# Performance work log

Hardware: AMD Instinct MI355X
Metric: run time of the kernel (lower is better)

The kernel has to match this reference:

```python
import jax, jax.numpy as jnp
import numpy as np

D = 256
N_EDGES = 8192
N_CORNERS = 4096


def setup_inputs() -> dict:
    key = jax.random.key(0)
    ks = jax.random.split(key, 8)
    scale = 1.0 / np.sqrt(D)
    return {
        "edge_pred": jax.random.uniform(ks[0], (N_EDGES,), dtype=jnp.float32),
        "edge_corner": jax.random.randint(ks[1], (N_EDGES, 2), 0, N_CORNERS, dtype=jnp.int64),
        "all_corners": jax.random.uniform(ks[2], (N_CORNERS, 2), dtype=jnp.float32),
        "edge_x": jax.random.normal(ks[3], (N_EDGES, D), dtype=jnp.float32),
        "image_x": jax.random.normal(ks[4], (1024,), dtype=jnp.float32),
        "W1": jax.random.normal(ks[5], (D, D), dtype=jnp.float32) * scale,
        "b1": jnp.zeros((D,), dtype=jnp.float32),
        "W2": jax.random.normal(ks[6], (D, D), dtype=jnp.float32) * scale,
        "b2": jnp.zeros((D,), dtype=jnp.float32),
        "W3": jax.random.normal(ks[7], (3 * D, D), dtype=jnp.float32) * scale,
        "b3": jnp.zeros((D,), dtype=jnp.float32),
    }


def _linear_block(x, W, b):
    # LinearBlock: Linear followed by ReLU
    return jax.nn.relu(x @ W + b)


def reference(edge_pred, edge_corner, all_corners, edge_x, image_x, W1, b1, W2, b2, W3, b3):
    # 'fully' branch of MPModule.forward. edge_pred/edge_corner/all_corners/image_x
    # are unused in this branch (kept for signature fidelity).
    e1 = _linear_block(edge_x, W1, b1)              # [N, D]
    # (e1.unsqueeze(1) * e1).mean(-1) == (e1 @ e1.T) / D   -> [N, N]
    sim1 = (e1 @ e1.T) / D
    e2 = _linear_block(edge_x, W2, b2)
    sim2 = (e2 @ e2.T) / D
    # (edge_x * sim.unsqueeze(-1)).sum(1) == sim @ edge_x  -> [N, D]
    agg1 = sim1 @ edge_x
    agg2 = sim2 @ edge_x
    cat = jnp.concatenate([edge_x, agg1, agg2], axis=-1)  # [N, 3D]
    out = _linear_block(cat, W3, b3)                      # [N, D]
    return out
```

## Files before the change

kernel.cpp:

```cpp
#include <hip/hip_runtime.h>

#define NE 8192
#define DD 256
#define NSPLIT 16

typedef __attribute__((ext_vector_type(8))) short short8;
typedef __attribute__((ext_vector_type(4))) short short4v;
typedef __attribute__((ext_vector_type(8))) __bf16 bf16x8;
typedef __attribute__((ext_vector_type(4))) float floatx4;

__device__ __forceinline__ unsigned short f2bf(float f) {
  union { float f; unsigned int i; } v; v.f = f;
  unsigned int r = v.i + 0x7fffu + ((v.i >> 16) & 1u);
  return (unsigned short)(r >> 16);
}

__device__ __forceinline__ floatx4 mfma_bf16(short8 a, short8 b, floatx4 c) {
  return __builtin_amdgcn_mfma_f32_16x16x32_bf16(
      __builtin_bit_cast(bf16x8, a), __builtin_bit_cast(bf16x8, b), c, 0, 0, 0);
}

__global__ __launch_bounds__(256, 2)
void e_gemm(const float* __restrict__ x,
            const float* __restrict__ W1, const float* __restrict__ b1,
            const float* __restrict__ W2, const float* __restrict__ b2,
            unsigned short* __restrict__ e1, unsigned short* __restrict__ e2,
            unsigned short* __restrict__ e1T, unsigned short* __restrict__ e2T,
            unsigned short* __restrict__ xT)
{
  __shared__ __align__(16) unsigned short smA[128 * 136];
  __shared__ __align__(16) unsigned short smB[64 * 136];
  const int T = threadIdx.x, lane = T & 63, wv = T >> 6;
  const int q = lane >> 4, r = lane & 15;
  const int z = blockIdx.z;
  const int col0 = blockIdx.x * 64, row0 = blockIdx.y * 128;
  const float* W = z ? W2 : W1;
  const float* bi = z ? b2 : b1;
  unsigned short* eo = z ? e2 : e1;
  unsigned short* eoT = z ? e2T : e1T;
  const bool emit = (z == 0) && ((int)blockIdx.x == (int)(blockIdx.y & 3));
  const int wr = (wv >> 1) * 64, wc = (wv & 1) * 32;

  floatx4 acc[4][2];
#pragma unroll
  for (int i = 0; i < 4; ++i)
#pragma unroll
    for (int j = 0; j < 2; ++j) acc[i][j] = (floatx4){0.f, 0.f, 0.f, 0.f};

  for (int kc = 0; kc < 256; kc += 128) {
#pragma unroll
    for (int p = 0; p < 16; ++p) {
      const int id = p * 256 + T, rr = id >> 5, k4 = (id & 31) * 4;
      floatx4 v = *(const floatx4*)&x[(size_t)(row0 + rr) * DD + kc + k4];
      short4v s;
#pragma unroll
      for (int c = 0; c < 4; ++c) s[c] = (short)f2bf(v[c]);
      *(short4v*)&smA[rr * 136 + k4] = s;
    }
#pragma unroll
    for (int p = 0; p < 2; ++p) {
      const int id = p * 256 + T, kb = id >> 4, n4 = id & 15;
      floatx4 wrow[4];
#pragma unroll
      for (int i = 0; i < 4; ++i)
        wrow[i] = *(const floatx4*)&W[(size_t)(kc + kb * 4 + i) * DD + col0 + n4 * 4];
#pragma unroll
      for (int s4 = 0; s4 < 4; ++s4) {
        const int c = (s4 + n4) & 3;
        short4v sv = {(short)f2bf(wrow[0][c]), (short)f2bf(wrow[1][c]),
                      (short)f2bf(wrow[2][c]), (short)f2bf(wrow[3][c])};
        *(short4v*)&smB[(n4 * 4 + c) * 136 + kb * 4] = sv;
      }
    }
    __syncthreads();
#pragma unroll
    for (int ks = 0; ks < 4; ++ks) {
      short8 af[4], bf[2];
#pragma unroll
      for (int i = 0; i < 4; ++i)
        af[i] = *(const short8*)&smA[(wr + i * 16 + r) * 136 + ks * 32 + q * 8];
#pragma unroll
      for (int j = 0; j < 2; ++j)
        bf[j] = *(const short8*)&smB[(wc + j * 16 + r) * 136 + ks * 32 + q * 8];
#pragma unroll
      for (int i = 0; i < 4; ++i)
#pragma unroll
        for (int j = 0; j < 2; ++j)
          acc[i][j] = mfma_bf16(af[i], bf[j], acc[i][j]);
    }
    if (emit) {
#pragma unroll
      for (int p = 0; p < 8; ++p) {
        const int id = p * 256 + T, kk = id >> 4, r8 = id & 15;
        short8 v;
#pragma unroll
        for (int i = 0; i < 8; ++i) v[i] = (short)smA[(r8 * 8 + i) * 136 + kk];
        *(short8*)&xT[(size_t)(kc + kk) * NE + row0 + r8 * 8] = v;
      }
    }
    __syncthreads();
  }

#pragma unroll
  for (int j = 0; j < 2; ++j) {
    const int col = col0 + wc + j * 16 + r;
    const float bv = bi[col];
#pragma unroll
    for (int i = 0; i < 4; ++i) {
      const int rowb = row0 + wr + i * 16 + q * 4;
      short4v tv;
#pragma unroll
      for (int t = 0; t < 4; ++t) {
        unsigned short h = f2bf(fmaxf(acc[i][j][t] + bv, 0.0f));
        tv[t] = (short)h;
        eo[(size_t)(rowb + t) * DD + col] = h;
      }
      *(short4v*)&eoT[(size_t)col * NE + rowb] = tv;
    }
  }
}

__global__ __launch_bounds__(256, 2)
void atb(const unsigned short* __restrict__ e1T, const unsigned short* __restrict__ e2T,
         const unsigned short* __restrict__ xT, float* __restrict__ P_T)
{
  __shared__ __align__(16) unsigned short smA[64 * 136];
  __shared__ __align__(16) unsigned short smB[64 * 136];
  const int T = threadIdx.x, lane = T & 63, wv = T >> 6;
  const int q = lane >> 4, r = lane & 15;
  const int m0 = (blockIdx.x >> 2) * 64, n0 = (blockIdx.x & 3) * 64;
  const int y = blockIdx.y, z = blockIdx.z;
  const int j0 = y * (NE / NSPLIT);
  const unsigned short* E = z ? e2T : e1T;
  float* P = P_T + (size_t)(z * NSPLIT + y) * 65536;

  floatx4 acc[4];
#pragma unroll
  for (int j = 0; j < 4; ++j) acc[j] = (floatx4){0.f, 0.f, 0.f, 0.f};

  for (int jc = 0; jc < NE / NSPLIT; jc += 128) {
#pragma unroll
    for (int p = 0; p < 4; ++p) {
      const int id = p * 256 + T, mm = id >> 4, j8 = (id & 15) * 8;
      *(short8*)&smA[mm * 136 + j8] =
          *(const short8*)&E[(size_t)(m0 + mm) * NE + j0 + jc + j8];
      *(short8*)&smB[mm * 136 + j8] =
          *(const short8*)&xT[(size_t)(n0 + mm) * NE + j0 + jc + j8];
    }
    __syncthreads();
#pragma unroll
    for (int ks = 0; ks < 4; ++ks) {
      short8 af = *(const short8*)&smA[(wv * 16 + r) * 136 + ks * 32 + q * 8];
#pragma unroll
      for (int j = 0; j < 4; ++j) {
        short8 bf = *(const short8*)&smB[(j * 16 + r) * 136 + ks * 32 + q * 8];
        acc[j] = mfma_bf16(af, bf, acc[j]);
      }
    }
    __syncthreads();
  }
#pragma unroll
  for (int j = 0; j < 4; ++j) {
    const int n = n0 + j * 16 + r;
    const int m = m0 + wv * 16 + q * 4;
    *(floatx4*)&P[(size_t)n * DD + m] = acc[j];
  }
}

__global__ void reduce_g(const float* __restrict__ P_T, float* __restrict__ G_T) {
  int idx = blockIdx.x * 256 + threadIdx.x;
  int z = idx >> 14, off = idx & 16383;
  const floatx4* Pp = (const floatx4*)P_T;
  floatx4 s = (floatx4){0.f, 0.f, 0.f, 0.f};
#pragma unroll
  for (int y = 0; y < NSPLIT; ++y)
    s += Pp[(size_t)(z * NSPLIT + y) * 16384 + off];
  ((floatx4*)G_T)[idx] = s;
}

__global__ __launch_bounds__(256, 2)
void h_mfma(const float* __restrict__ G_T, const float* __restrict__ W3,
            unsigned short* __restrict__ H1t, unsigned short* __restrict__ H2t)
{
  __shared__ __align__(16) unsigned short smA[64 * 136];
  __shared__ __align__(16) unsigned short smB[64 * 136];
  const int T = threadIdx.x, lane = T & 63, wv = T >> 6;
  const int q = lane >> 4, r = lane & 15;
  const int z = blockIdx.z;
  const int me0 = (blockIdx.x >> 2) * 64, m30 = (blockIdx.x & 3) * 64;
  const float* G = G_T + (size_t)z * 65536;
  unsigned short* Ht = z ? H2t : H1t;
  const int woff = 256 + z * 256;

  floatx4 acc[4];
#pragma unroll
  for (int j = 0; j < 4; ++j) acc[j] = (floatx4){0.f, 0.f, 0.f, 0.f};

  for (int lc = 0; lc < 256; lc += 128) {
#pragma unroll
    for (int p = 0; p < 2; ++p) {
      const int id = p * 256 + T, lb = id >> 4, e4 = id & 15;
      floatx4 grow[4], wrow[4];
#pragma unroll
      for (int i = 0; i < 4; ++i) {
        grow[i] = *(const floatx4*)&G[(size_t)(lc + lb * 4 + i) * DD + me0 + e4 * 4];
        wrow[i] = *(const floatx4*)&W3[(size_t)(woff + lc + lb * 4 + i) * DD + m30 + e4 * 4];
      }
#pragma unroll
      for (int s4 = 0; s4 < 4; ++s4) {
        const int c = (s4 + e4) & 3;
        short4v ga = {(short)f2bf(grow[0][c] * 0.00390625f),
                      (short)f2bf(grow[1][c] * 0.00390625f),
                      (short)f2bf(grow[2][c] * 0.00390625f),
                      (short)f2bf(grow[3][c] * 0.00390625f)};
        short4v wa = {(short)f2bf(wrow[0][c]), (short)f2bf(wrow[1][c]),
                      (short)f2bf(wrow[2][c]), (short)f2bf(wrow[3][c])};
        *(short4v*)&smA[(e4 * 4 + c) * 136 + lb * 4] = ga;
        *(short4v*)&smB[(e4 * 4 + c) * 136 + lb * 4] = wa;
      }
    }
    __syncthreads();
#pragma unroll
    for (int ks = 0; ks < 4; ++ks) {
      short8 af = *(const short8*)&smA[(wv * 16 + r) * 136 + ks * 32 + q * 8];
#pragma unroll
      for (int j = 0; j < 4; ++j) {
        short8 bf = *(const short8*)&smB[(j * 16 + r) * 136 + ks * 32 + q * 8];
        acc[j] = mfma_bf16(af, bf, acc[j]);
      }
    }
    __syncthreads();
  }
#pragma unroll
  for (int j = 0; j < 4; ++j) {
    const int m3 = m30 + j * 16 + r;
    const int me = me0 + wv * 16 + q * 4;
    short4v v;
#pragma unroll
    for (int i = 0; i < 4; ++i) v[i] = (short)f2bf(acc[j][i]);
    *(short4v*)&Ht[(size_t)m3 * DD + me] = v;
  }
}

__global__ __launch_bounds__(256, 2)
void out_gemm(const float* __restrict__ x,
              const unsigned short* __restrict__ e1, const unsigned short* __restrict__ e2,
              const float* __restrict__ W3,
              const unsigned short* __restrict__ H1t, const unsigned short* __restrict__ H2t,
              const float* __restrict__ b3, float* __restrict__ out)
{
  __shared__ __align__(16) unsigned short smA[64 * 136];
  __shared__ __align__(16) unsigned short smB[64 * 136];
  const int T = threadIdx.x, lane = T & 63, wv = T >> 6;
  const int q = lane >> 4, r = lane & 15;
  const int col0 = blockIdx.x * 64, row0 = blockIdx.y * 64;

  floatx4 acc[4];
#pragma unroll
  for (int j = 0; j < 4; ++j) acc[j] = (floatx4){0.f, 0.f, 0.f, 0.f};

  for (int s = 0; s < 3; ++s) {
    for (int kc = 0; kc < 256; kc += 128) {
      if (s == 0) {
#pragma unroll
        for (int p = 0; p < 8; ++p) {
          const int id = p * 256 + T, rr = id >> 5, k4 = (id & 31) * 4;
          floatx4 v = *(const floatx4*)&x[(size_t)(row0 + rr) * DD + kc + k4];
          short4v sv;
#pragma unroll
          for (int c = 0; c < 4; ++c) sv[c] = (short)f2bf(v[c]);
          *(short4v*)&smA[rr * 136 + k4] = sv;
        }
#pragma unroll
        for (int p = 0; p < 2; ++p) {
          const int id = p * 256 + T, kb = id >> 4, n4 = id & 15;
          floatx4 wrow[4];
#pragma unroll
          for (int i = 0; i < 4; ++i)
            wrow[i] = *(const floatx4*)&W3[(size_t)(kc + kb * 4 + i) * DD + col0 + n4 * 4];
#pragma unroll
          for (int s4 = 0; s4 < 4; ++s4) {
            const int c = (s4 + n4) & 3;
            short4v sv = {(short)f2bf(wrow[0][c]), (short)f2bf(wrow[1][c]),
                          (short)f2bf(wrow[2][c]), (short)f2bf(wrow[3][c])};
            *(short4v*)&smB[(n4 * 4 + c) * 136 + kb * 4] = sv;
          }
        }
      } else {
        const unsigned short* E = (s == 1) ? e1 : e2;
        const unsigned short* Hs = (s == 1) ? H1t : H2t;
#pragma unroll
        for (int p = 0; p < 4; ++p) {
          const int id = p * 256 + T, rr = id >> 4, j8 = (id & 15) * 8;
          *(short8*)&smA[rr * 136 + j8] =
              *(const short8*)&E[(size_t)(row0 + rr) * DD + kc + j8];
          *(short8*)&smB[rr * 136 + j8] =
              *(const short8*)&Hs[(size_t)(col0 + rr) * DD + kc + j8];
        }
      }
      __syncthreads();
#pragma unroll
      for (int ks = 0; ks < 4; ++ks) {
        short8 af = *(const short8*)&smA[(wv * 16 + r) * 136 + ks * 32 + q * 8];
#pragma unroll
        for (int j = 0; j < 4; ++j) {
          short8 bf = *(const short8*)&smB[(j * 16 + r) * 136 + ks * 32 + q * 8];
          acc[j] = mfma_bf16(af, bf, acc[j]);
        }
      }
      __syncthreads();
    }
  }
#pragma unroll
  for (int j = 0; j < 4; ++j) {
    const int col = col0 + j * 16 + r;
    const float bv = b3[col];
    const int rowb = row0 + wv * 16 + q * 4;
#pragma unroll
    for (int t = 0; t < 4; ++t)
      out[(size_t)(rowb + t) * DD + col] = fmaxf(acc[j][t] + bv, 0.0f);
  }
}

extern "C" void kernel_launch(void* const* d_in, const int* in_sizes, int n_in,
                              void* d_out, int out_size, void* d_ws, size_t ws_size,
                              hipStream_t stream) {
  (void)in_sizes; (void)n_in; (void)out_size; (void)ws_size;
  const float* x  = (const float*)d_in[3];
  const float* W1 = (const float*)d_in[5];
  const float* b1 = (const float*)d_in[6];
  const float* W2 = (const float*)d_in[7];
  const float* b2 = (const float*)d_in[8];
  const float* W3 = (const float*)d_in[9];
  const float* b3 = (const float*)d_in[10];
  float* out = (float*)d_out;

  char* ws = (char*)d_ws;
  const size_t MB = 1u << 20;
  const size_t KB = 1u << 10;
  unsigned short* e1  = (unsigned short*)ws;
  unsigned short* e2  = (unsigned short*)(ws + 4 * MB);
  unsigned short* e1T = (unsigned short*)(ws + 8 * MB);
  unsigned short* e2T = (unsigned short*)(ws + 12 * MB);
  unsigned short* xT  = (unsigned short*)(ws + 16 * MB);
  unsigned short* H1t = (unsigned short*)(ws + 20 * MB);
  unsigned short* H2t = (unsigned short*)(ws + 20 * MB + 128 * KB);
  float* G_T          = (float*)(ws + 20 * MB + 256 * KB);
  float* P_T          = (float*)(ws + 21 * MB);

  e_gemm<<<dim3(4, 64, 2), 256, 0, stream>>>(x, W1, b1, W2, b2, e1, e2, e1T, e2T, xT);
  atb<<<dim3(16, NSPLIT, 2), 256, 0, stream>>>(e1T, e2T, xT, P_T);
  reduce_g<<<128, 256, 0, stream>>>(P_T, G_T);
  h_mfma<<<dim3(16, 1, 2), 256, 0, stream>>>(G_T, W3, H1t, H2t);
  out_gemm<<<dim3(4, 128), 256, 0, stream>>>(x, e1, e2, W3, H1t, H2t, b3, out);
}
```

Before: 137.1 us.

## Fuse W1/W2 projections per block, double split-K and raise occupancy hints

e_gemm now computes both e1 and e2 in one block, sharing the bf16-converted x tile across the W1 and W2 products. This halves x loads and conversions, and the tile shrinks to 64 rows over a 4x128 grid. NSPLIT rises from 16 to 32 for more parallelism in the atb split-K stage, and launch bounds rise on several kernels to allow more resident blocks. The larger partial-sum buffer means more reduction work and more workspace traffic, and the doubled P_T size may overflow the workspace region beyond G_T.

```diff
diff --git a/kernel.cpp b/kernel.cpp
--- a/kernel.cpp
+++ b/kernel.cpp
@@ -2,7 +2,7 @@
 
 #define NE 8192
 #define DD 256
-#define NSPLIT 16
+#define NSPLIT 32
 
 typedef __attribute__((ext_vector_type(8))) short short8;
 typedef __attribute__((ext_vector_type(4))) short short4v;
@@ -20,7 +20,7 @@
       __builtin_bit_cast(bf16x8, a), __builtin_bit_cast(bf16x8, b), c, 0, 0, 0);
 }
 
-__global__ __launch_bounds__(256, 2)
+__global__ __launch_bounds__(256, 3)
 void e_gemm(const float* __restrict__ x,
             const float* __restrict__ W1, const float* __restrict__ b1,
             const float* __restrict__ W2, const float* __restrict__ b2,
@@ -28,28 +28,24 @@
             unsigned short* __restrict__ e1T, unsigned short* __restrict__ e2T,
             unsigned short* __restrict__ xT)
 {
-  __shared__ __align__(16) unsigned short smA[128 * 136];
-  __shared__ __align__(16) unsigned short smB[64 * 136];
+  __shared__ __align__(16) unsigned short smA[64 * 136];
+  __shared__ __align__(16) unsigned short smB1[64 * 136];
+  __shared__ __align__(16) unsigned short smB2[64 * 136];
   const int T = threadIdx.x, lane = T & 63, wv = T >> 6;
   const int q = lane >> 4, r = lane & 15;
-  const int z = blockIdx.z;
-  const int col0 = blockIdx.x * 64, row0 = blockIdx.y * 128;
-  const float* W = z ? W2 : W1;
-  const float* bi = z ? b2 : b1;
-  unsigned short* eo = z ? e2 : e1;
-  unsigned short* eoT = z ? e2T : e1T;
-  const bool emit = (z == 0) && ((int)blockIdx.x == (int)(blockIdx.y & 3));
-  const int wr = (wv >> 1) * 64, wc = (wv & 1) * 32;
-
-  floatx4 acc[4][2];
-#pragma unroll
-  for (int i = 0; i < 4; ++i)
-#pragma unroll
-    for (int j = 0; j < 2; ++j) acc[i][j] = (floatx4){0.f, 0.f, 0.f, 0.f};
+  const int col0 = blockIdx.x * 64, row0 = blockIdx.y * 64;
+  const bool emit = ((int)blockIdx.x == (int)(blockIdx.y & 3));
+
+  floatx4 acc1[4], acc2[4];
+#pragma unroll
+  for (int j = 0; j < 4; ++j) {
+    acc1[j] = (floatx4){0.f, 0.f, 0.f, 0.f};
+    acc2[j] = (floatx4){0.f, 0.f, 0.f, 0.f};
+  }
 
   for (int kc = 0; kc < 256; kc += 128) {
 #pragma unroll
-    for (int p = 0; p < 16; ++p) {
+    for (int p = 0; p < 8; ++p) {
       const int id = p * 256 + T, rr = id >> 5, k4 = (id & 31) * 4;
       floatx4 v = *(const floatx4*)&x[(size_t)(row0 + rr) * DD + kc + k4];
       short4v s;
@@ -60,67 +56,68 @@
 #pragma unroll
     for (int p = 0; p < 2; ++p) {
       const int id = p * 256 + T, kb = id >> 4, n4 = id & 15;
-      floatx4 wrow[4];
-#pragma unroll
-      for (int i = 0; i < 4; ++i)
-        wrow[i] = *(const floatx4*)&W[(size_t)(kc + kb * 4 + i) * DD + col0 + n4 * 4];
+      floatx4 w1r[4], w2r[4];
+#pragma unroll
+      for (int i = 0; i < 4; ++i) {
+        w1r[i] = *(const floatx4*)&W1[(size_t)(kc + kb * 4 + i) * DD + col0 + n4 * 4];
+        w2r[i] = *(const floatx4*)&W2[(size_t)(kc + kb * 4 + i) * DD + col0 + n4 * 4];
+      }
 #pragma unroll
       for (int s4 = 0; s4 < 4; ++s4) {
         const int c = (s4 + n4) & 3;
-        short4v sv = {(short)f2bf(wrow[0][c]), (short)f2bf(wrow[1][c]),
-                      (short)f2bf(wrow[2][c]), (short)f2bf(wrow[3][c])};
-        *(short4v*)&smB[(n4 * 4 + c) * 136 + kb * 4] = sv;
+        short4v s1 = {(short)f2bf(w1r[0][c]), (short)f2bf(w1r[1][c]),
+                      (short)f2bf(w1r[2][c]), (short)f2bf(w1r[3][c])};
+        short4v s2 = {(short)f2bf(w2r[0][c]), (short)f2bf(w2r[1][c]),
+                      (short)f2bf(w2r[2][c]), (short)f2bf(w2r[3][c])};
+        *(short4v*)&smB1[(n4 * 4 + c) * 136 + kb * 4] = s1;
+        *(short4v*)&smB2[(n4 * 4 + c) * 136 + kb * 4] = s2;
       }
     }
     __syncthreads();
 #pragma unroll
     for (int ks = 0; ks < 4; ++ks) {
-      short8 af[4], bf[2];
-#pragma unroll
-      for (int i = 0; i < 4; ++i)
-        af[i] = *(const short8*)&smA[(wr + i * 16 + r) * 136 + ks * 32 + q * 8];
-#pragma unroll
-      for (int j = 0; j < 2; ++j)
-        bf[j] = *(const short8*)&smB[(wc + j * 16 + r) * 136 + ks * 32 + q * 8];
-#pragma unroll
-      for (int i = 0; i < 4; ++i)
-#pragma unroll
-        for (int j = 0; j < 2; ++j)
-          acc[i][j] = mfma_bf16(af[i], bf[j], acc[i][j]);
+      short8 af = *(const short8*)&smA[(wv * 16 + r) * 136 + ks * 32 + q * 8];
+#pragma unroll
+      for (int j = 0; j < 4; ++j) {
+        short8 b1f = *(const short8*)&smB1[(j * 16 + r) * 136 + ks * 32 + q * 8];
+        short8 b2f = *(const short8*)&smB2[(j * 16 + r) * 136 + ks * 32 + q * 8];
+        acc1[j] = mfma_bf16(af, b1f, acc1[j]);
+        acc2[j] = mfma_bf16(af, b2f, acc2[j]);
+      }
     }
     if (emit) {
 #pragma unroll
-      for (int p = 0; p < 8; ++p) {
-        const int id = p * 256 + T, kk = id >> 4, r8 = id & 15;
+      for (int p = 0; p < 4; ++p) {
+        const int id = p * 256 + T, kk = id >> 3, r8 = (id & 7) * 8;
         short8 v;
 #pragma unroll
-        for (int i = 0; i < 8; ++i) v[i] = (short)smA[(r8 * 8 + i) * 136 + kk];
-        *(short8*)&xT[(size_t)(kc + kk) * NE + row0 + r8 * 8] = v;
-      }
-    }
-    __syncthreads();
-  }
-
-#pragma unroll
-  for (int j = 0; j < 2; ++j) {
-    const int col = col0 + wc + j * 16 + r;
-    const float bv = bi[col];
-#pragma unroll
-    for (int i = 0; i < 4; ++i) {
-      const int rowb = row0 + wr + i * 16 + q * 4;
-      short4v tv;
-#pragma unroll
-      for (int t = 0; t < 4; ++t) {
-        unsigned short h = f2bf(fmaxf(acc[i][j][t] + bv, 0.0f));
-        tv[t] = (short)h;
-        eo[(size_t)(rowb + t) * DD + col] = h;
-      }
-      *(short4v*)&eoT[(size_t)col * NE + rowb] = tv;
-    }
-  }
-}
-
-__global__ __launch_bounds__(256, 2)
+        for (int i = 0; i < 8; ++i) v[i] = (short)smA[(r8 + i) * 136 + kk];
+        *(short8*)&xT[(size_t)(kc + kk) * NE + row0 + r8] = v;
+      }
+    }
+    __syncthreads();
+  }
+
+#pragma unroll
+  for (int j = 0; j < 4; ++j) {
+    const int col = col0 + j * 16 + r;
+    const int rowb = row0 + wv * 16 + q * 4;
+    const float b1v = b1[col], b2v = b2[col];
+    short4v t1, t2;
+#pragma unroll
+    for (int t = 0; t < 4; ++t) {
+      unsigned short h1 = f2bf(fmaxf(acc1[j][t] + b1v, 0.0f));
+      unsigned short h2 = f2bf(fmaxf(acc2[j][t] + b2v, 0.0f));
+      t1[t] = (short)h1; t2[t] = (short)h2;
+      e1[(size_t)(rowb + t) * DD + col] = h1;
+      e2[(size_t)(rowb + t) * DD + col] = h2;
+    }
+    *(short4v*)&e1T[(size_t)col * NE + rowb] = t1;
+    *(short4v*)&e2T[(size_t)col * NE + rowb] = t2;
+  }
+}
+
+__global__ __launch_bounds__(256, 4)
 void atb(const unsigned short* __restrict__ e1T, const unsigned short* __restrict__ e2T,
          const unsigned short* __restrict__ xT, float* __restrict__ P_T)
 {
@@ -242,7 +239,7 @@
   }
 }
 
-__global__ __launch_bounds__(256, 2)
+__global__ __launch_bounds__(256, 4)
 void out_gemm(const float* __restrict__ x,
               const unsigned short* __restrict__ e1, const unsigned short* __restrict__ e2,
               const float* __restrict__ W3,
@@ -348,7 +345,7 @@
   float* G_T          = (float*)(ws + 20 * MB + 256 * KB);
   float* P_T          = (float*)(ws + 21 * MB);
 
-  e_gemm<<<dim3(4, 64, 2), 256, 0, stream>>>(x, W1, b1, W2, b2, e1, e2, e1T, e2T, xT);
+  e_gemm<<<dim3(4, 128), 256, 0, stream>>>(x, W1, b1, W2, b2, e1, e2, e1T, e2T, xT);
   atb<<<dim3(16, NSPLIT, 2), 256, 0, stream>>>(e1T, e2T, xT, P_T);
   reduce_g<<<128, 256, 0, stream>>>(P_T, G_T);
   h_mfma<<<dim3(16, 1, 2), 256, 0, stream>>>(G_T, W3, H1t, H2t);
```

Result: no change. 134.7 us (-1.7%).
